# Optimization experiments

Measured on AMD Instinct MI355X. Metric: run time of the kernel, lower is better.

## Reference

```python
import jax, jax.numpy as jnp
import numpy as np

DIM, D_STATE, D_CONV, EXPAND = 1024, 16, 4, 2
D_INNER = EXPAND * DIM
DT_RANK = (DIM + 15) // 16  # 64
B_SZ, L_SEQ = 2, 1024
EPS = 1e-5


def setup_inputs() -> dict:
    key = jax.random.key(0)
    ks = jax.random.split(key, 10)
    s_in = 1.0 / np.sqrt(DIM)
    s_xp = 1.0 / np.sqrt(D_INNER)
    s_dt = 1.0 / np.sqrt(DT_RANK)
    return {
        "x": jax.random.normal(ks[0], (B_SZ, L_SEQ, DIM), jnp.float32),
        "norm_w": jnp.ones((DIM,), jnp.float32),
        "in_proj_w": jax.random.normal(ks[1], (2 * D_INNER, DIM), jnp.float32) * s_in,
        "conv_w": jax.random.normal(ks[2], (D_INNER, 1, D_CONV), jnp.float32) * 0.5,
        "conv_b": jnp.zeros((D_INNER,), jnp.float32),
        "x_proj_w": jax.random.normal(ks[3], (DT_RANK + 2 * D_STATE, D_INNER), jnp.float32) * s_xp,
        "dt_proj_w": jax.random.normal(ks[4], (D_INNER, DT_RANK), jnp.float32) * s_dt,
        "dt_proj_b": jax.random.uniform(ks[5], (D_INNER,), jnp.float32, -4.0, -1.0),
        # S4D-real init: A = -[1..d_state] per inner channel
        "A_log": jnp.log(jnp.tile(jnp.arange(1, D_STATE + 1, dtype=jnp.float32), (D_INNER, 1))),
        "D_param": jnp.ones((D_INNER,), jnp.float32),
        "out_proj_w": jax.random.normal(ks[6], (DIM, D_INNER), jnp.float32) * s_xp,
    }


def _mamba_block(x, norm_w, in_proj_w, conv_w, conv_b, x_proj_w,
                 dt_proj_w, dt_proj_b, A_log, D_param, out_proj_w):
    # RMSNorm
    xn = x * jax.lax.rsqrt(jnp.mean(x * x, axis=-1, keepdims=True) + EPS) * norm_w
    # input projection -> (B, L, 2*d_inner)
    xz = jnp.einsum("bld,ed->ble", xn, in_proj_w)
    xi, z = jnp.split(xz, 2, axis=-1)
    # depthwise causal conv1d over time
    xc = jax.lax.conv_general_dilated(
        xi.transpose(0, 2, 1),                    # (B, d_inner, L)
        conv_w,                                    # (d_inner, 1, d_conv)
        window_strides=(1,),
        padding=[(D_CONV - 1, 0)],
        dimension_numbers=("NCH", "OIH", "NCH"),
        feature_group_count=D_INNER,
    ) + conv_b[None, :, None]
    u = jax.nn.silu(xc.transpose(0, 2, 1))         # (B, L, d_inner)
    # data-dependent SSM parameters
    x_dbl = jnp.einsum("bld,ed->ble", u, x_proj_w)
    dt, Bm, Cm = jnp.split(x_dbl, [DT_RANK, DT_RANK + D_STATE], axis=-1)
    delta = jax.nn.softplus(jnp.einsum("blr,dr->bld", dt, dt_proj_w) + dt_proj_b)
    A = -jnp.exp(A_log)                            # (d_inner, d_state)

    def step(h, inp):
        delta_t, B_t, C_t, u_t = inp               # (B,di), (B,ds), (B,ds), (B,di)
        dA = jnp.exp(delta_t[..., None] * A)       # (B, di, ds)
        dBu = (delta_t * u_t)[..., None] * B_t[:, None, :]
        h = dA * h + dBu
        y = jnp.einsum("bds,bs->bd", h, C_t)
        return h, y

    h0 = jnp.zeros((x.shape[0], D_INNER, D_STATE), x.dtype)
    inputs = (delta.swapaxes(0, 1), Bm.swapaxes(0, 1), Cm.swapaxes(0, 1), u.swapaxes(0, 1))
    _, ys = jax.lax.scan(step, h0, inputs)
    y = ys.swapaxes(0, 1) + u * D_param            # (B, L, d_inner)
    y = y * jax.nn.silu(z)
    out = jnp.einsum("ble,de->bld", y, out_proj_w)
    return x + out                                  # residual


def reference(x, norm_w, in_proj_w, conv_w, conv_b, x_proj_w,
              dt_proj_w, dt_proj_b, A_log, D_param, out_proj_w):
    return _mamba_block(x, norm_w, in_proj_w, conv_w, conv_b, x_proj_w,
                        dt_proj_w, dt_proj_b, A_log, D_param, out_proj_w)
```

## Files before the change

kernel.cpp:

```cpp
#include <hip/hip_runtime.h>
#include <math.h>

#define DIMX 1024
#define D_STATE 16
#define D_INNER 2048
#define DT_RANK 64
#define B_SZ 2
#define L_SEQ 1024
#define NTOK (B_SZ * L_SEQ)
#define EPSR 1e-5f
#define NC 32
#define LC 32
#define NCH (B_SZ * D_INNER)
#define NLANE (NCH * D_STATE)
#define LOG2E 1.44269504f

typedef __attribute__((ext_vector_type(8))) short bf16x8;
typedef __attribute__((ext_vector_type(4))) int   i32x4;
typedef __attribute__((ext_vector_type(4))) float f32x4;
typedef __attribute__((ext_vector_type(4))) unsigned short u16x4;

__device__ __forceinline__ unsigned short f2b(float f) {
    unsigned int u = __builtin_bit_cast(unsigned int, f);
    u += 0x7fffu + ((u >> 16) & 1u);
    return (unsigned short)(u >> 16);
}
__device__ __forceinline__ float b2f(unsigned short h) {
    unsigned int u = ((unsigned int)h) << 16;
    return __builtin_bit_cast(float, u);
}
__device__ __forceinline__ float lo2f(unsigned int v) {
    return __builtin_bit_cast(float, v << 16);
}
__device__ __forceinline__ float hi2f(unsigned int v) {
    return __builtin_bit_cast(float, v & 0xffff0000u);
}
__device__ __forceinline__ void gload16(const void* g, void* l) {
    __builtin_amdgcn_global_load_lds(
        (const __attribute__((address_space(1))) unsigned int*)g,
        (__attribute__((address_space(3))) unsigned int*)l, 16, 0, 0);
}

#define N1C (2 * D_INNER * DIMX / 4)
#define N2C (96 * D_INNER / 4)
#define N3C (D_INNER * DT_RANK / 4)
#define N4C (DIMX * D_INNER / 4)
__global__ void f2b_all(const float* __restrict__ w_in, const float* __restrict__ w_x,
                        const float* __restrict__ w_dt, const float* __restrict__ w_out,
                        unsigned short* __restrict__ o_in, unsigned short* __restrict__ o_x,
                        unsigned short* __restrict__ o_dt, unsigned short* __restrict__ o_out) {
    int i = blockIdx.x * 256 + threadIdx.x;
    const float* src; unsigned short* dst; int j;
    if (i < N1C)                       { src = w_in;  dst = o_in;  j = i; }
    else if (i < N1C + N2C)            { src = w_x;   dst = o_x;   j = i - N1C; }
    else if (i < N1C + N2C + N3C)      { src = w_dt;  dst = o_dt;  j = i - N1C - N2C; }
    else if (i < N1C + N2C + N3C + N4C){ src = w_out; dst = o_out; j = i - N1C - N2C - N3C; }
    else return;
    f32x4 v = *(const f32x4*)(src + (size_t)j * 4);
    unsigned short o[4];
#pragma unroll
    for (int k = 0; k < 4; ++k) o[k] = f2b(v[k]);
    *(unsigned long long*)(dst + (size_t)j * 4) = *(unsigned long long*)o;
}

__global__ void rmsnorm_kernel(const float* __restrict__ x, const float* __restrict__ w,
                               unsigned short* __restrict__ xnb) {
    int row = blockIdx.x;
    const float* xr = x + (size_t)row * DIMX;
    unsigned short* outr = xnb + (size_t)row * DIMX;
    int t = threadIdx.x;
    float v[4];
    float ss = 0.f;
#pragma unroll
    for (int i = 0; i < 4; ++i) { v[i] = xr[t + i * 256]; ss += v[i] * v[i]; }
#pragma unroll
    for (int off = 32; off > 0; off >>= 1) ss += __shfl_down(ss, off);
    __shared__ float red[4];
    if ((t & 63) == 0) red[t >> 6] = ss;
    __syncthreads();
    float tot = red[0] + red[1] + red[2] + red[3];
    float scale = rsqrtf(tot * (1.f / DIMX) + EPSR);
#pragma unroll
    for (int i = 0; i < 4; ++i) outr[t + i * 256] = f2b(v[i] * scale * w[t + i * 256]);
}

__global__ __launch_bounds__(256) void conv_silu_tr(
    const unsigned short* __restrict__ xiT, const float* __restrict__ cw,
    const float* __restrict__ cb, unsigned short* __restrict__ u_row) {
    __shared__ unsigned int xs[67 * 65];
    __shared__ unsigned int ob[64 * 65];
    const int t0 = blockIdx.x * 64;
    const int d0 = blockIdx.y * 64;
    const int bstart = t0 & ~(L_SEQ - 1);
    const int tid = threadIdx.x;
    for (int task = tid; task < 576; task += 256) {
        int d = task & 63, c = task >> 6;
        int tc = t0 - 8 + c * 8;
        int tl = tc < 0 ? 0 : tc;
        i32x4 v = *(const i32x4*)(xiT + (size_t)(d0 + d) * NTOK + tl);
        const unsigned short* vs = (const unsigned short*)&v;
#pragma unroll
        for (int i = 0; i < 8; ++i) {
            int t = tc + i;
            int row = t - (t0 - 3);
            if (row >= 0 && row < 67) {
                float xv = (t >= bstart) ? b2f(vs[i]) : 0.f;
                xs[row * 65 + d] = __builtin_bit_cast(unsigned int, xv);
            }
        }
    }
    __syncthreads();
    {
        const int dl = tid & 63, tr = tid >> 6;
        const int d = d0 + dl, lt0 = tr * 16;
        const float w0 = cw[d * 4 + 0], w1 = cw[d * 4 + 1], w2 = cw[d * 4 + 2], w3 = cw[d * 4 + 3];
        const float bias = cb[d];
        float x0 = __builtin_bit_cast(float, xs[(lt0 + 0) * 65 + dl]);
        float x1 = __builtin_bit_cast(float, xs[(lt0 + 1) * 65 + dl]);
        float x2 = __builtin_bit_cast(float, xs[(lt0 + 2) * 65 + dl]);
#pragma unroll
        for (int i = 0; i < 16; ++i) {
            float x3 = __builtin_bit_cast(float, xs[(lt0 + 3 + i) * 65 + dl]);
            float a = bias + w0 * x0 + w1 * x1 + w2 * x2 + w3 * x3;
            ob[(lt0 + i) * 65 + dl] = f2b(a / (1.f + __expf(-a)));
            x0 = x1; x1 = x2; x2 = x3;
        }
    }
    __syncthreads();
#pragma unroll
    for (int it = 0; it < 2; ++it) {
        int k = tid + it * 256;
        int t = k >> 3, d8 = (k & 7) * 8;
        unsigned short o[8];
#pragma unroll
        for (int j = 0; j < 8; ++j) o[j] = (unsigned short)ob[t * 65 + d8 + j];
        *(i32x4*)(u_row + (size_t)(t0 + t) * D_INNER + d0 + d8) = *(const i32x4*)o;
    }
}

template <int EPI>
__global__ __launch_bounds__(256) void gemm_mfma(
    const unsigned short* __restrict__ A, const unsigned short* __restrict__ B,
    void* __restrict__ C, void* __restrict__ C2,
    int M, int N, int K, int lda, int ldb, int ldc,
    const float* __restrict__ bias, const float* __restrict__ res,
    const float* __restrict__ aux) {
    __shared__ unsigned short As[128 * 32];
    __shared__ unsigned short Bs[128 * 32];
    const int tid = threadIdx.x;
    const int m0 = blockIdx.y * 128, n0 = blockIdx.x * 128;
    const int lane = tid & 63, wave = tid >> 6;
    const int wr = (wave >> 1) * 64, wc = (wave & 1) * 64;
    const int fr = lane & 15, fk = (lane >> 4) * 8;
    const int kspan = K / gridDim.z;
    const int kb = blockIdx.z * kspan;
    const int srow = lane >> 2, sc8 = (lane & 3) * 8;
    f32x4 acc[4][4] = {};
    for (int k0 = kb; k0 < kb + kspan; k0 += 32) {
#pragma unroll
        for (int i = 0; i < 2; ++i) {
            int q = wave + 4 * i;
            int row = q * 16 + srow;
            gload16(A + (size_t)(m0 + row) * lda + k0 + sc8, (unsigned short*)As + q * 512);
            gload16(B + (size_t)(n0 + row) * ldb + k0 + sc8, (unsigned short*)Bs + q * 512);
        }
        __syncthreads();
        bf16x8 af[4], bfr[4];
#pragma unroll
        for (int i = 0; i < 4; ++i) af[i]  = *(const bf16x8*)&As[(wr + i * 16 + fr) * 32 + fk];
#pragma unroll
        for (int j = 0; j < 4; ++j) bfr[j] = *(const bf16x8*)&Bs[(wc + j * 16 + fr) * 32 + fk];
#pragma unroll
        for (int i = 0; i < 4; ++i)
#pragma unroll
            for (int j = 0; j < 4; ++j)
                acc[i][j] = __builtin_amdgcn_mfma_f32_16x16x32_bf16(af[i], bfr[j], acc[i][j], 0, 0, 0);
        __syncthreads();
    }
    const int er = (lane >> 4) * 4;
    if (EPI == 3) {
        unsigned short* xiT = (unsigned short*)C;
        unsigned short* zR  = (unsigned short*)C2;
#pragma unroll
        for (int i = 0; i < 4; ++i)
#pragma unroll
            for (int j = 0; j < 4; ++j) {
                int row0 = m0 + wr + i * 16 + er;
                int col = n0 + wc + j * 16 + fr;
                if (col < D_INNER) {
                    unsigned short o[4];
#pragma unroll
                    for (int r = 0; r < 4; ++r) o[r] = f2b(acc[i][j][r]);
                    *(unsigned long long*)(xiT + (size_t)col * NTOK + row0) = *(unsigned long long*)o;
                } else {
#pragma unroll
                    for (int r = 0; r < 4; ++r)
                        zR[(size_t)(row0 + r) * D_INNER + col - D_INNER] = f2b(acc[i][j][r]);
                }
            }
    } else if (EPI == 1) {
        const unsigned short* uR = (const unsigned short*)res;
        unsigned int* dduP = (unsigned int*)C;
        unsigned short* uDP = (unsigned short*)C2;
#pragma unroll
        for (int i = 0; i < 4; ++i)
#pragma unroll
            for (int j = 0; j < 4; ++j) {
                int row0 = m0 + wr + i * 16 + er;
                int col = n0 + wc + j * 16 + fr;
                float bb = bias[col];
                float Dv = aux[col];
#pragma unroll
                for (int r = 0; r < 4; ++r) {
                    size_t idx = (size_t)(row0 + r) * D_INNER + col;
                    float t = acc[i][j][r] + bb;
                    float v = fmaxf(t, 0.f) + log1pf(expf(-fabsf(t)));
                    float uf = b2f(uR[idx]);
                    dduP[idx] = ((unsigned)f2b(v)) | (((unsigned)f2b(v * uf)) << 16);
                    uDP[idx] = f2b(uf * Dv);
                }
            }
    } else {
        float* Cs = (float*)C + (size_t)blockIdx.z * M * ldc;
#pragma unroll
        for (int i = 0; i < 4; ++i)
#pragma unroll
            for (int j = 0; j < 4; ++j) {
                int col = n0 + wc + j * 16 + fr;
                if (col < N) {
#pragma unroll
                    for (int r = 0; r < 4; ++r) {
                        int row = m0 + wr + i * 16 + er + r;
                        Cs[(size_t)row * ldc + col] = acc[i][j][r];
                    }
                }
            }
    }
}

__global__ void combine_residual(const float* __restrict__ part, const float* __restrict__ x,
                                 float* __restrict__ out) {
    int i = blockIdx.x * 256 + threadIdx.x;
    f32x4 s = *(const f32x4*)(x + (size_t)i * 4);
#pragma unroll
    for (int z = 0; z < 4; ++z)
        s += *(const f32x4*)(part + (size_t)z * NTOK * DIMX + (size_t)i * 4);
    *(f32x4*)(out + (size_t)i * 4) = s;
}

__global__ void xproj_combine(const float* __restrict__ xp, unsigned short* __restrict__ xdbl_b,
                              float* __restrict__ B_T, float* __restrict__ C_T) {
    int row = blockIdx.x;
    int col = threadIdx.x;
    if (col >= 96) return;
    float s = 0.f;
#pragma unroll
    for (int p = 0; p < 8; ++p) s += xp[(size_t)p * NTOK * 96 + (size_t)row * 96 + col];
    if (col < 64) xdbl_b[row * 64 + col] = f2b(s);
    else if (col < 80) B_T[(size_t)(col - 64) * NTOK + row] = s;
    else C_T[(size_t)(col - 80) * NTOK + row] = s;
}


__global__ __launch_bounds__(256) void scan_pass1(
    const unsigned int* __restrict__ ddu, const float* __restrict__ B_T,
    const float* __restrict__ A_log, float* __restrict__ hl, float* __restrict__ Pc) {
    __shared__ float bs[LC][20];
    const int tid = threadIdx.x;
    const int chunk = blockIdx.x;
    const int gchan = blockIdx.y * 256 + tid;
    const int b = gchan >> 11, d = gchan & (D_INNER - 1);
    const int tb = b * L_SEQ + chunk * LC;
    for (int v = tid; v < LC * 16; v += 256) {
        int t = v & (LC - 1), s = v >> 5;
        bs[t][s] = B_T[(size_t)s * NTOK + tb + t];
    }
    __syncthreads();
    float A2[D_STATE], h[D_STATE];
    const float* al = A_log + d * D_STATE;
#pragma unroll
    for (int s = 0; s < D_STATE; ++s) { A2[s] = -__expf(al[s]) * LOG2E; h[s] = 0.f; }
    float dsum = 0.f;
    const unsigned int* pd = ddu + (size_t)tb * D_INNER + d;
    unsigned int pf[8];
#pragma unroll
    for (int t = 0; t < 8; ++t) pf[t] = pd[(size_t)t * D_INNER];
#pragma unroll
    for (int t = 0; t < LC; ++t) {
        unsigned int v = pf[t & 7];
        if (t + 8 < LC) pf[t & 7] = pd[(size_t)(t + 8) * D_INNER];
        float dl = lo2f(v), du = hi2f(v);
        dsum += dl;
#pragma unroll
        for (int i = 0; i < 4; ++i) {
            f32x4 bv = *(const f32x4*)&bs[t][4 * i];
#pragma unroll
            for (int q = 0; q < 4; ++q) {
                int s = 4 * i + q;
                float e = exp2f(dl * A2[s]);
                h[s] = e * h[s] + du * bv[q];
            }
        }
    }
    float* ph = hl + (size_t)chunk * NLANE + (size_t)gchan * D_STATE;
    float* pp = Pc + (size_t)chunk * NLANE + (size_t)gchan * D_STATE;
#pragma unroll
    for (int q = 0; q < 4; ++q) {
        f32x4 hv = {h[4 * q], h[4 * q + 1], h[4 * q + 2], h[4 * q + 3]};
        f32x4 pv = {exp2f(dsum * A2[4 * q]),     exp2f(dsum * A2[4 * q + 1]),
                    exp2f(dsum * A2[4 * q + 2]), exp2f(dsum * A2[4 * q + 3])};
        *(f32x4*)(ph + 4 * q) = hv;
        *(f32x4*)(pp + 4 * q) = pv;
    }
}

__global__ __launch_bounds__(256) void scan_pass2(const float* __restrict__ hl,
                                                  const float* __restrict__ Pc,
                                                  float* __restrict__ hi) {
    int gid = blockIdx.x * 256 + threadIdx.x;
    float h = 0.f;
    hi[gid] = 0.f;
#pragma unroll
    for (int c = 1; c < NC; ++c) {
        h = hl[(size_t)(c - 1) * NLANE + gid] + Pc[(size_t)(c - 1) * NLANE + gid] * h;
        hi[(size_t)c * NLANE + gid] = h;
    }
}

__global__ __launch_bounds__(256) void scan_pass3(
    const unsigned int* __restrict__ ddu, const float* __restrict__ B_T,
    const float* __restrict__ C_T, const unsigned short* __restrict__ uD,
    const unsigned short* __restrict__ z_row, const float* __restrict__ A_log,
    const float* __restrict__ hi, unsigned short* __restrict__ y_row) {
    __shared__ float bcs[LC][36];
    const int tid = threadIdx.x;
    const int chunk = blockIdx.x;
    const int gchan = blockIdx.y * 256 + tid;
    const int b = gchan >> 11, d = gchan & (D_INNER - 1);
    const int tb = b * L_SEQ + chunk * LC;
    for (int v = tid; v < LC * 32; v += 256) {
        int t = v & (LC - 1), q = v >> 5;
        bcs[t][q] = (q < 16) ? B_T[(size_t)q * NTOK + tb + t]
                             : C_T[(size_t)(q - 16) * NTOK + tb + t];
    }
    __syncthreads();
    float A2[D_STATE], h[D_STATE];
    const float* al = A_log + d * D_STATE;
#pragma unroll
    for (int s = 0; s < D_STATE; ++s) A2[s] = -__expf(al[s]) * LOG2E;
    const float* ph = hi + (size_t)chunk * NLANE + (size_t)gchan * D_STATE;
#pragma unroll
    for (int q = 0; q < 4; ++q) {
        f32x4 hv = *(const f32x4*)(ph + 4 * q);
#pragma unroll
        for (int r = 0; r < 4; ++r) h[4 * q + r] = hv[r];
    }
    const unsigned int* pd = ddu + (size_t)tb * D_INNER + d;
    const unsigned short* pu = uD + (size_t)tb * D_INNER + d;
    const unsigned short* pz = z_row + (size_t)tb * D_INNER + d;
    unsigned short* py = y_row + (size_t)tb * D_INNER + d;
    unsigned int pf[4];
    unsigned short pfu[4], pfz[4];
#pragma unroll
    for (int t = 0; t < 4; ++t) {
        pf[t] = pd[(size_t)t * D_INNER];
        pfu[t] = pu[(size_t)t * D_INNER];
        pfz[t] = pz[(size_t)t * D_INNER];
    }
#pragma unroll
    for (int t = 0; t < LC; ++t) {
        unsigned int v = pf[t & 3];
        float uDv = b2f(pfu[t & 3]);
        float zz = b2f(pfz[t & 3]);
        if (t + 4 < LC) {
            pf[t & 3] = pd[(size_t)(t + 4) * D_INNER];
            pfu[t & 3] = pu[(size_t)(t + 4) * D_INNER];
            pfz[t & 3] = pz[(size_t)(t + 4) * D_INNER];
        }
        float dl = lo2f(v), du = hi2f(v);
        float y0 = 0.f, y1 = 0.f, y2 = 0.f, y3 = 0.f;
#pragma unroll
        for (int i = 0; i < 4; ++i) {
            f32x4 bv = *(const f32x4*)&bcs[t][4 * i];
            f32x4 cv = *(const f32x4*)&bcs[t][16 + 4 * i];
#pragma unroll
            for (int q = 0; q < 4; ++q) {
                int s = 4 * i + q;
                float e = exp2f(dl * A2[s]);
                h[s] = e * h[s] + du * bv[q];
                float yv = h[s] * cv[q];
                if (q == 0) y0 += yv;
                else if (q == 1) y1 += yv;
                else if (q == 2) y2 += yv;
                else y3 += yv;
            }
        }
        float y = (y0 + y1) + (y2 + y3);
        float yy = y + uDv;
        py[(size_t)t * D_INNER] = f2b(yy * (zz / (1.f + __expf(-zz))));
    }
}

extern "C" void kernel_launch(void* const* d_in, const int* in_sizes, int n_in,
                              void* d_out, int out_size, void* d_ws, size_t ws_size,
                              hipStream_t stream) {
    const float* x          = (const float*)d_in[0];
    const float* norm_w     = (const float*)d_in[1];
    const float* in_proj_w  = (const float*)d_in[2];
    const float* conv_w     = (const float*)d_in[3];
    const float* conv_b     = (const float*)d_in[4];
    const float* x_proj_w   = (const float*)d_in[5];
    const float* dt_proj_w  = (const float*)d_in[6];
    const float* dt_proj_b  = (const float*)d_in[7];
    const float* A_log      = (const float*)d_in[8];
    const float* D_param    = (const float*)d_in[9];
    const float* out_proj_w = (const float*)d_in[10];
    float* out = (float*)d_out;

    char* p = (char*)d_ws;
    unsigned short* xi_T  = (unsigned short*)p; p += (size_t)D_INNER * NTOK * 2;
    unsigned short* z_row = (unsigned short*)p; p += (size_t)NTOK * D_INNER * 2;
    unsigned int*   ddu   = (unsigned int*)p;   p += (size_t)NTOK * D_INNER * 4;
    unsigned short* u_row = (unsigned short*)p; p += (size_t)NTOK * D_INNER * 2;
    unsigned short* uD    = (unsigned short*)p; p += (size_t)NTOK * D_INNER * 2;
    unsigned short* y_row = (unsigned short*)p; p += (size_t)NTOK * D_INNER * 2;
    unsigned short* xdbl_b = (unsigned short*)p; p += (size_t)NTOK * 64 * 2;
    float* B_T = (float*)p;  p += (size_t)D_STATE * NTOK * 4;
    float* C_T = (float*)p;  p += (size_t)D_STATE * NTOK * 4;
    unsigned short* xn_b = (unsigned short*)p; p += (size_t)NTOK * DIMX * 2;
    unsigned short* w_in_b  = (unsigned short*)p; p += (size_t)2 * D_INNER * DIMX * 2;
    unsigned short* w_x_b   = (unsigned short*)p; p += (size_t)96 * D_INNER * 2;
    unsigned short* w_dt_b  = (unsigned short*)p; p += (size_t)D_INNER * DT_RANK * 2;
    unsigned short* w_out_b = (unsigned short*)p; p += (size_t)DIMX * D_INNER * 2;

    float* xp_part = (float*)y_row;
    float* hl = (float*)u_row;
    float* Pc = (float*)w_in_b;
    float* hi = (float*)xi_T;
    float* out_part = (float*)ddu;

    f2b_all<<<(N1C + N2C + N3C + N4C + 255) / 256, 256, 0, stream>>>(
        in_proj_w, x_proj_w, dt_proj_w, out_proj_w, w_in_b, w_x_b, w_dt_b, w_out_b);

    rmsnorm_kernel<<<NTOK, 256, 0, stream>>>(x, norm_w, xn_b);
    gemm_mfma<3><<<dim3(32, 16), 256, 0, stream>>>(xn_b, w_in_b, xi_T, z_row,
        NTOK, 2 * D_INNER, DIMX, DIMX, DIMX, NTOK, nullptr, nullptr, nullptr);
    conv_silu_tr<<<dim3(NTOK / 64, D_INNER / 64), 256, 0, stream>>>(
        xi_T, conv_w, conv_b, u_row);
    gemm_mfma<0><<<dim3(1, 16, 8), 256, 0, stream>>>(u_row, w_x_b, xp_part, nullptr,
        NTOK, 96, D_INNER, D_INNER, D_INNER, 96, nullptr, nullptr, nullptr);
    xproj_combine<<<NTOK, 128, 0, stream>>>(xp_part, xdbl_b, B_T, C_T);
    gemm_mfma<1><<<dim3(16, 16), 256, 0, stream>>>(xdbl_b, w_dt_b, ddu, uD,
        NTOK, D_INNER, DT_RANK, 64, DT_RANK, D_INNER, dt_proj_b, (const float*)u_row, D_param);
    scan_pass1<<<dim3(NC, NCH / 256), 256, 0, stream>>>(ddu, B_T, A_log, hl, Pc);
    scan_pass2<<<NLANE / 256, 256, 0, stream>>>(hl, Pc, hi);
    scan_pass3<<<dim3(NC, NCH / 256), 256, 0, stream>>>(ddu, B_T, C_T, uD, z_row, A_log, hi, y_row);
    gemm_mfma<0><<<dim3(8, 16, 4), 256, 0, stream>>>(y_row, w_out_b, out_part, nullptr,
        NTOK, DIMX, D_INNER, D_INNER, D_INNER, DIMX, nullptr, nullptr, nullptr);
    combine_residual<<<NTOK * DIMX / 4 / 256, 256, 0, stream>>>(out_part, x, out);
}
```

Baseline: 187.8 us.

## Fuse prep kernels, store xi row-major, cheaper softplus, fewer out-proj K splits

Merges the weight bf16 conversion and RMSNorm into one launch, which removes a kernel launch. The in-proj GEMM now writes xi row-major instead of transposed, and the conv kernel is rewritten to read rows with vector loads. Softplus switches to fast __logf/__expf intrinsics, which may cost a little accuracy. The out-proj split-K drops from 4 to 2, so the combine step reads less partial data, at the cost of less parallelism in that GEMM.

```diff
diff --git a/kernel.cpp b/kernel.cpp
--- a/kernel.cpp
+++ b/kernel.cpp
@@ -45,47 +45,50 @@
 #define N2C (96 * D_INNER / 4)
 #define N3C (D_INNER * DT_RANK / 4)
 #define N4C (DIMX * D_INNER / 4)
-__global__ void f2b_all(const float* __restrict__ w_in, const float* __restrict__ w_x,
-                        const float* __restrict__ w_dt, const float* __restrict__ w_out,
-                        unsigned short* __restrict__ o_in, unsigned short* __restrict__ o_x,
-                        unsigned short* __restrict__ o_dt, unsigned short* __restrict__ o_out) {
-    int i = blockIdx.x * 256 + threadIdx.x;
-    const float* src; unsigned short* dst; int j;
-    if (i < N1C)                       { src = w_in;  dst = o_in;  j = i; }
-    else if (i < N1C + N2C)            { src = w_x;   dst = o_x;   j = i - N1C; }
-    else if (i < N1C + N2C + N3C)      { src = w_dt;  dst = o_dt;  j = i - N1C - N2C; }
-    else if (i < N1C + N2C + N3C + N4C){ src = w_out; dst = o_out; j = i - N1C - N2C - N3C; }
-    else return;
-    f32x4 v = *(const f32x4*)(src + (size_t)j * 4);
-    unsigned short o[4];
-#pragma unroll
-    for (int k = 0; k < 4; ++k) o[k] = f2b(v[k]);
-    *(unsigned long long*)(dst + (size_t)j * 4) = *(unsigned long long*)o;
-}
-
-__global__ void rmsnorm_kernel(const float* __restrict__ x, const float* __restrict__ w,
-                               unsigned short* __restrict__ xnb) {
-    int row = blockIdx.x;
-    const float* xr = x + (size_t)row * DIMX;
-    unsigned short* outr = xnb + (size_t)row * DIMX;
-    int t = threadIdx.x;
-    float v[4];
-    float ss = 0.f;
-#pragma unroll
-    for (int i = 0; i < 4; ++i) { v[i] = xr[t + i * 256]; ss += v[i] * v[i]; }
-#pragma unroll
-    for (int off = 32; off > 0; off >>= 1) ss += __shfl_down(ss, off);
-    __shared__ float red[4];
-    if ((t & 63) == 0) red[t >> 6] = ss;
-    __syncthreads();
-    float tot = red[0] + red[1] + red[2] + red[3];
-    float scale = rsqrtf(tot * (1.f / DIMX) + EPSR);
-#pragma unroll
-    for (int i = 0; i < 4; ++i) outr[t + i * 256] = f2b(v[i] * scale * w[t + i * 256]);
-}
-
-__global__ __launch_bounds__(256) void conv_silu_tr(
-    const unsigned short* __restrict__ xiT, const float* __restrict__ cw,
+#define NWCONV ((N1C + N2C + N3C + N4C + 255) / 256)
+__global__ __launch_bounds__(256) void prep_kernel(
+    const float* __restrict__ w_in, const float* __restrict__ w_x,
+    const float* __restrict__ w_dt, const float* __restrict__ w_out,
+    const float* __restrict__ x, const float* __restrict__ norm_w,
+    unsigned short* __restrict__ o_in, unsigned short* __restrict__ o_x,
+    unsigned short* __restrict__ o_dt, unsigned short* __restrict__ o_out,
+    unsigned short* __restrict__ xnb) {
+    if ((int)blockIdx.x < NWCONV) {
+        int i = blockIdx.x * 256 + threadIdx.x;
+        const float* src; unsigned short* dst; int j;
+        if (i < N1C)                        { src = w_in;  dst = o_in;  j = i; }
+        else if (i < N1C + N2C)             { src = w_x;   dst = o_x;   j = i - N1C; }
+        else if (i < N1C + N2C + N3C)       { src = w_dt;  dst = o_dt;  j = i - N1C - N2C; }
+        else if (i < N1C + N2C + N3C + N4C) { src = w_out; dst = o_out; j = i - N1C - N2C - N3C; }
+        else return;
+        f32x4 v = *(const f32x4*)(src + (size_t)j * 4);
+        unsigned short o[4];
+#pragma unroll
+        for (int k = 0; k < 4; ++k) o[k] = f2b(v[k]);
+        *(unsigned long long*)(dst + (size_t)j * 4) = *(unsigned long long*)o;
+    } else {
+        int row = blockIdx.x - NWCONV;
+        const float* xr = x + (size_t)row * DIMX;
+        unsigned short* outr = xnb + (size_t)row * DIMX;
+        int t = threadIdx.x;
+        float v[4];
+        float ss = 0.f;
+#pragma unroll
+        for (int i = 0; i < 4; ++i) { v[i] = xr[t + i * 256]; ss += v[i] * v[i]; }
+#pragma unroll
+        for (int off = 32; off > 0; off >>= 1) ss += __shfl_down(ss, off);
+        __shared__ float red[4];
+        if ((t & 63) == 0) red[t >> 6] = ss;
+        __syncthreads();
+        float tot = red[0] + red[1] + red[2] + red[3];
+        float scale = rsqrtf(tot * (1.f / DIMX) + EPSR);
+#pragma unroll
+        for (int i = 0; i < 4; ++i) outr[t + i * 256] = f2b(v[i] * scale * norm_w[t + i * 256]);
+    }
+}
+
+__global__ __launch_bounds__(256) void conv_silu_row(
+    const unsigned short* __restrict__ xiR, const float* __restrict__ cw,
     const float* __restrict__ cb, unsigned short* __restrict__ u_row) {
     __shared__ unsigned int xs[67 * 65];
     __shared__ unsigned int ob[64 * 65];
@@ -93,20 +96,18 @@
     const int d0 = blockIdx.y * 64;
     const int bstart = t0 & ~(L_SEQ - 1);
     const int tid = threadIdx.x;
-    for (int task = tid; task < 576; task += 256) {
-        int d = task & 63, c = task >> 6;
-        int tc = t0 - 8 + c * 8;
-        int tl = tc < 0 ? 0 : tc;
-        i32x4 v = *(const i32x4*)(xiT + (size_t)(d0 + d) * NTOK + tl);
-        const unsigned short* vs = (const unsigned short*)&v;
-#pragma unroll
-        for (int i = 0; i < 8; ++i) {
-            int t = tc + i;
-            int row = t - (t0 - 3);
-            if (row >= 0 && row < 67) {
-                float xv = (t >= bstart) ? b2f(vs[i]) : 0.f;
-                xs[row * 65 + d] = __builtin_bit_cast(unsigned int, xv);
-            }
+    for (int task = tid; task < 536; task += 256) {
+        int row = task >> 3, c8 = (task & 7) * 8;
+        int t = t0 - 3 + row;
+        if (t >= bstart) {
+            i32x4 v = *(const i32x4*)(xiR + (size_t)t * D_INNER + d0 + c8);
+            const unsigned short* vs = (const unsigned short*)&v;
+#pragma unroll
+            for (int i = 0; i < 8; ++i)
+                xs[row * 65 + c8 + i] = __builtin_bit_cast(unsigned int, b2f(vs[i]));
+        } else {
+#pragma unroll
+            for (int i = 0; i < 8; ++i) xs[row * 65 + c8 + i] = 0u;
         }
     }
     __syncthreads();
@@ -179,7 +180,7 @@
     }
     const int er = (lane >> 4) * 4;
     if (EPI == 3) {
-        unsigned short* xiT = (unsigned short*)C;
+        unsigned short* xiR = (unsigned short*)C;
         unsigned short* zR  = (unsigned short*)C2;
 #pragma unroll
         for (int i = 0; i < 4; ++i)
@@ -187,16 +188,13 @@
             for (int j = 0; j < 4; ++j) {
                 int row0 = m0 + wr + i * 16 + er;
                 int col = n0 + wc + j * 16 + fr;
-                if (col < D_INNER) {
-                    unsigned short o[4];
-#pragma unroll
-                    for (int r = 0; r < 4; ++r) o[r] = f2b(acc[i][j][r]);
-                    *(unsigned long long*)(xiT + (size_t)col * NTOK + row0) = *(unsigned long long*)o;
-                } else {
-#pragma unroll
-                    for (int r = 0; r < 4; ++r)
-                        zR[(size_t)(row0 + r) * D_INNER + col - D_INNER] = f2b(acc[i][j][r]);
-                }
+                unsigned short* dst;
+                int colm;
+                if (col < D_INNER) { dst = xiR; colm = col; }
+                else               { dst = zR;  colm = col - D_INNER; }
+#pragma unroll
+                for (int r = 0; r < 4; ++r)
+                    dst[(size_t)(row0 + r) * D_INNER + colm] = f2b(acc[i][j][r]);
             }
     } else if (EPI == 1) {
         const unsigned short* uR = (const unsigned short*)res;
@@ -214,7 +212,7 @@
                 for (int r = 0; r < 4; ++r) {
                     size_t idx = (size_t)(row0 + r) * D_INNER + col;
                     float t = acc[i][j][r] + bb;
-                    float v = fmaxf(t, 0.f) + log1pf(expf(-fabsf(t)));
+                    float v = fmaxf(t, 0.f) + __logf(1.f + __expf(-fabsf(t)));
                     float uf = b2f(uR[idx]);
                     dduP[idx] = ((unsigned)f2b(v)) | (((unsigned)f2b(v * uf)) << 16);
                     uDP[idx] = f2b(uf * Dv);
@@ -243,7 +241,7 @@
     int i = blockIdx.x * 256 + threadIdx.x;
     f32x4 s = *(const f32x4*)(x + (size_t)i * 4);
 #pragma unroll
-    for (int z = 0; z < 4; ++z)
+    for (int z = 0; z < 2; ++z)
         s += *(const f32x4*)(part + (size_t)z * NTOK * DIMX + (size_t)i * 4);
     *(f32x4*)(out + (size_t)i * 4) = s;
 }
@@ -418,12 +416,12 @@
     float* out = (float*)d_out;
 
     char* p = (char*)d_ws;
-    unsigned short* xi_T  = (unsigned short*)p; p += (size_t)D_INNER * NTOK * 2;
-    unsigned short* z_row = (unsigned short*)p; p += (size_t)NTOK * D_INNER * 2;
-    unsigned int*   ddu   = (unsigned int*)p;   p += (size_t)NTOK * D_INNER * 4;
-    unsigned short* u_row = (unsigned short*)p; p += (size_t)NTOK * D_INNER * 2;
-    unsigned short* uD    = (unsigned short*)p; p += (size_t)NTOK * D_INNER * 2;
-    unsigned short* y_row = (unsigned short*)p; p += (size_t)NTOK * D_INNER * 2;
+    unsigned short* xi_row = (unsigned short*)p; p += (size_t)NTOK * D_INNER * 2;
+    unsigned short* z_row  = (unsigned short*)p; p += (size_t)NTOK * D_INNER * 2;
+    unsigned int*   ddu    = (unsigned int*)p;   p += (size_t)NTOK * D_INNER * 4;
+    unsigned short* u_row  = (unsigned short*)p; p += (size_t)NTOK * D_INNER * 2;
+    unsigned short* uD     = (unsigned short*)p; p += (size_t)NTOK * D_INNER * 2;
+    unsigned short* y_row  = (unsigned short*)p; p += (size_t)NTOK * D_INNER * 2;
     unsigned short* xdbl_b = (unsigned short*)p; p += (size_t)NTOK * 64 * 2;
     float* B_T = (float*)p;  p += (size_t)D_STATE * NTOK * 4;
     float* C_T = (float*)p;  p += (size_t)D_STATE * NTOK * 4;
@@ -436,17 +434,16 @@
     float* xp_part = (float*)y_row;
     float* hl = (float*)u_row;
     float* Pc = (float*)w_in_b;
-    float* hi = (float*)xi_T;
+    float* hi = (float*)xi_row;
     float* out_part = (float*)ddu;
 
-    f2b_all<<<(N1C + N2C + N3C + N4C + 255) / 256, 256, 0, stream>>>(
-        in_proj_w, x_proj_w, dt_proj_w, out_proj_w, w_in_b, w_x_b, w_dt_b, w_out_b);
-
-    rmsnorm_kernel<<<NTOK, 256, 0, stream>>>(x, norm_w, xn_b);
-    gemm_mfma<3><<<dim3(32, 16), 256, 0, stream>>>(xn_b, w_in_b, xi_T, z_row,
-        NTOK, 2 * D_INNER, DIMX, DIMX, DIMX, NTOK, nullptr, nullptr, nullptr);
-    conv_silu_tr<<<dim3(NTOK / 64, D_INNER / 64), 256, 0, stream>>>(
-        xi_T, conv_w, conv_b, u_row);
+    prep_kernel<<<NWCONV + NTOK, 256, 0, stream>>>(
+        in_proj_w, x_proj_w, dt_proj_w, out_proj_w, x, norm_w,
+        w_in_b, w_x_b, w_dt_b, w_out_b, xn_b);
+    gemm_mfma<3><<<dim3(32, 16), 256, 0, stream>>>(xn_b, w_in_b, xi_row, z_row,
+        NTOK, 2 * D_INNER, DIMX, DIMX, DIMX, D_INNER, nullptr, nullptr, nullptr);
+    conv_silu_row<<<dim3(NTOK / 64, D_INNER / 64), 256, 0, stream>>>(
+        xi_row, conv_w, conv_b, u_row);
     gemm_mfma<0><<<dim3(1, 16, 8), 256, 0, stream>>>(u_row, w_x_b, xp_part, nullptr,
         NTOK, 96, D_INNER, D_INNER, D_INNER, 96, nullptr, nullptr, nullptr);
     xproj_combine<<<NTOK, 128, 0, stream>>>(xp_part, xdbl_b, B_T, C_T);
@@ -455,7 +452,7 @@
     scan_pass1<<<dim3(NC, NCH / 256), 256, 0, stream>>>(ddu, B_T, A_log, hl, Pc);
     scan_pass2<<<NLANE / 256, 256, 0, stream>>>(hl, Pc, hi);
     scan_pass3<<<dim3(NC, NCH / 256), 256, 0, stream>>>(ddu, B_T, C_T, uD, z_row, A_log, hi, y_row);
-    gemm_mfma<0><<<dim3(8, 16, 4), 256, 0, stream>>>(y_row, w_out_b, out_part, nullptr,
+    gemm_mfma<0><<<dim3(8, 16, 2), 256, 0, stream>>>(y_row, w_out_b, out_part, nullptr,
         NTOK, DIMX, D_INNER, D_INNER, D_INNER, DIMX, nullptr, nullptr, nullptr);
     combine_residual<<<NTOK * DIMX / 4 / 256, 256, 0, stream>>>(out_part, x, out);
 }
```

New measurement: 174.2 us (median of 2 runs). 1.08x faster.
